# Performance work log

Measured on AMD Instinct MI355X. Metric: run time of the kernel, lower is better.

Reference implementation:

```python
import jax, jax.numpy as jnp
import numpy as np

MAX_SPAN_LENGTH = 4


def setup_inputs() -> dict:
    key = jax.random.key(0)
    ks = jax.random.split(key, 6)
    B, S, H, E = 8, 2048, 768, 32
    hidden_states = jax.random.normal(ks[0], (B, S, H), jnp.float32)
    topic_vector = jax.random.normal(ks[1], (B, H), jnp.float32)
    text_mask = jnp.ones((B, S), dtype=bool)
    length_embedding = jax.random.normal(ks[2], (MAX_SPAN_LENGTH + 1, E), jnp.float32) * 0.02
    W1 = jax.random.normal(ks[3], (3 * H + E, H), jnp.float32) * 0.02
    b1 = jnp.zeros((H,), jnp.float32)
    W2 = jax.random.normal(ks[4], (H, 1), jnp.float32) * 0.02
    b2 = jnp.zeros((1,), jnp.float32)
    return {"hidden_states": hidden_states, "topic_vector": topic_vector,
            "text_mask": text_mask, "length_embedding": length_embedding,
            "W1": W1, "b1": b1, "W2": W2, "b2": b2}


def reference(hidden_states, topic_vector, text_mask, length_embedding, W1, b1, W2, b2):
    B, S, H = hidden_states.shape
    L = MAX_SPAN_LENGTH
    NEG = jnp.float32(-jnp.inf)

    # Static span grid (text_mask is full): span k = (start, start+off), off in [0, L)
    offs = jnp.arange(L)
    starts = jnp.repeat(jnp.arange(S), L)          # [N] with N = S*L
    ends = starts + jnp.tile(offs, S)              # [N]
    valid = ends < S                               # pad spans running off the end
    ends_c = jnp.minimum(ends, S - 1)
    lengths = jnp.tile(offs + 1, S)                # [N] in [1, L]

    start_v = hidden_states[:, starts, :]          # [B,N,H] gather span starts
    end_v = hidden_states[:, ends_c, :]            # [B,N,H] gather span ends
    len_v = length_embedding[lengths]              # [N,E]
    N = starts.shape[0]
    topic = jnp.broadcast_to(topic_vector[:, None, :], (B, N, H))
    feats = jnp.concatenate(
        [topic, start_v, end_v, jnp.broadcast_to(len_v[None], (B, N, len_v.shape[-1]))],
        axis=-1)                                   # [B,N,3H+E]

    h = jax.nn.gelu(feats @ W1 + b1, approximate=False)   # [B,N,H]
    span_scores = (h @ W2)[..., 0] + b2[0]                 # [B,N]
    span_scores = jnp.where(valid[None, :], span_scores, NEG)

    # Project span scores back to tokens via masked max over covering spans
    tok = jnp.arange(S)
    cover = (tok[None, :] >= starts[:, None]) & (tok[None, :] <= ends_c[:, None])  # [N,S]
    token_scores = jnp.max(
        jnp.where(cover[None, :, :], span_scores[:, :, None], NEG), axis=1)       # [B,S]
    token_scores = jnp.where(text_mask, token_scores, NEG)
    return token_scores, span_scores
```

## Files before the change

kernel.cpp:

```cpp
#include <hip/hip_runtime.h>
#include <math.h>

#define B 8
#define S 2048
#define H 768
#define E 32
#define L 4
#define M (B*S)
#define NCOL (2*H)
#define K 768

#define NEG_SENTINEL (-1.0e30f)

typedef float v4f __attribute__((ext_vector_type(4)));
typedef short v8s __attribute__((ext_vector_type(8)));
typedef _Float16 v8h __attribute__((ext_vector_type(8)));
typedef _Float16 v4h __attribute__((ext_vector_type(4)));

__device__ __forceinline__ void bfsplit(float f, unsigned short& h, unsigned short& l) {
  unsigned u = __float_as_uint(f);
  unsigned r = u + 0x7FFF + ((u >> 16) & 1);
  h = (unsigned short)(r >> 16);
  float fh = __uint_as_float(r & 0xFFFF0000u);
  float fl = f - fh;
  unsigned u2 = __float_as_uint(fl);
  unsigned r2 = u2 + 0x7FFF + ((u2 >> 16) & 1);
  l = (unsigned short)(r2 >> 16);
}
__device__ __forceinline__ void split4(float4 f, uint2& h, uint2& l) {
  unsigned short h0,h1,h2,h3,l0,l1,l2,l3;
  bfsplit(f.x,h0,l0); bfsplit(f.y,h1,l1); bfsplit(f.z,h2,l2); bfsplit(f.w,h3,l3);
  h.x = (unsigned)h0 | ((unsigned)h1 << 16); h.y = (unsigned)h2 | ((unsigned)h3 << 16);
  l.x = (unsigned)l0 | ((unsigned)l1 << 16); l.y = (unsigned)l2 | ((unsigned)l3 << 16);
}

__device__ __forceinline__ float gelu_f(float x) {
  float y  = x * 0.70710678118654752f;
  float ay = fabsf(y);
  float t  = __builtin_amdgcn_rcpf(fmaf(0.3275911f, ay, 1.0f));
  float poly = t * fmaf(t, fmaf(t, fmaf(t, fmaf(t, 1.061405429f, -1.453152027f),
                                        1.421413741f), -0.284496736f), 0.254829592f);
  float e  = __expf(-y * y);
  float er = 1.0f - poly * e;
  er = __builtin_copysignf(er, y);
  return 0.5f * x * (1.0f + er);
}


#define SPLITA_BLOCKS 6144
#define CONVW_BLOCKS 288
#define MISC_BLOCKS 36
#define TOPICW_BLOCKS 768

__global__ __launch_bounds__(256) void prep(
    const float* __restrict__ A, const float* __restrict__ W1,
    const float* __restrict__ lenemb, const float* __restrict__ b1,
    _Float16* __restrict__ Af, _Float16* __restrict__ Wf,
    float* __restrict__ topicW, float* __restrict__ lenbase)
{
  __shared__ float t[64][65];
  int bx = blockIdx.x;
  if (bx < SPLITA_BLOCKS) {
    int c = bx * 256 + threadIdx.x;
    int mr = c & 15;
    int cell = c >> 4;
    int kc = cell % 96;
    int m16 = cell / 96;
    int m = m16 * 16 + mr;
    int k0 = kc * 8;
    float4 f0 = *(const float4*)(A + (size_t)m * K + k0);
    float4 f1 = *(const float4*)(A + (size_t)m * K + k0 + 4);
    v8h hv;
    hv[0] = (_Float16)f0.x; hv[1] = (_Float16)f0.y;
    hv[2] = (_Float16)f0.z; hv[3] = (_Float16)f0.w;
    hv[4] = (_Float16)f1.x; hv[5] = (_Float16)f1.y;
    hv[6] = (_Float16)f1.z; hv[7] = (_Float16)f1.w;
    *(v8h*)(Af + (size_t)c * 8) = hv;
  } else if (bx < SPLITA_BLOCKS + CONVW_BLOCKS) {
    int blk = bx - SPLITA_BLOCKS;
    int kb = blk % (K / 64);
    int nb = blk / (K / 64);
    int k0 = kb * 64, n0 = nb * 64;
    int tn = threadIdx.x & 63, tk = threadIdx.x >> 6;
    int n = n0 + tn;
    const float* src = (n < H) ? (W1 + (size_t)(H + k0) * H + n)
                               : (W1 + (size_t)(2 * H + k0) * H + (n - H));
    #pragma unroll
    for (int s = 0; s < 16; s++) {
      int kk = tk + s * 4;
      t[kk][tn] = src[(size_t)kk * H];
    }
    __syncthreads();
    int tkk = threadIdx.x & 63, tnn = threadIdx.x >> 6;
    #pragma unroll
    for (int s = 0; s < 16; s++) {
      int nn = tnn + s * 4;
      float v = t[tkk][nn];
      int n_g = n0 + nn;
      int kk_g = k0 + tkk;
      size_t go = ((size_t)((n_g >> 4) * 96 + (kk_g >> 3)) * 16 + (n_g & 15)) * 8
                + (kk_g & 7);
      Wf[go] = (_Float16)v;
    }
  } else {
    int idx = (bx - SPLITA_BLOCKS - CONVW_BLOCKS) * 256 + threadIdx.x;
    if (idx < L * H) {
      int l = idx / H, h = idx % H;
      float s = b1[h];
      const float* le = lenemb + (size_t)(l + 1) * E;
      #pragma unroll
      for (int e = 0; e < E; e++)
        s = fmaf(le[e], W1[(size_t)(3 * H + e) * H + h], s);
      lenbase[idx] = s;
    } else if (idx < L * H + B * H) {
      topicW[idx - L * H] = 0.f;
    }
  }
}

__global__ __launch_bounds__(256) void gemm_mfma(
    const _Float16* __restrict__ Af, const _Float16* __restrict__ Wf,
    const float* __restrict__ topic, const float* __restrict__ W1,
    float* __restrict__ topicW,
    _Float16* __restrict__ P, _Float16* __restrict__ Q)
{
  __shared__ float red[4][64];
  int tid = threadIdx.x, lane = tid & 63, wv = tid >> 6;
  int f = blockIdx.x;

  if (f >= (M / 128) * (NCOL / 128)) {
    int tw = f - (M / 128) * (NCOL / 128);
    int b = tw / 96;
    int r = tw % 96;
    int h0 = (r / 8) * 64;
    int kc0 = (r % 8) * 96;
    int hcol = tid & 63, ksub = tid >> 6;
    const float* tp = topic + (size_t)b * H;
    float s = 0.f;
    #pragma unroll
    for (int i = 0; i < 24; i++) {
      int k = kc0 + ksub * 24 + i;
      s = fmaf(tp[k], W1[(size_t)k * H + h0 + hcol], s);
    }
    red[ksub][hcol] = s;
    __syncthreads();
    if (tid < 64) {
      float tot = red[0][tid] + red[1][tid] + red[2][tid] + red[3][tid];
      atomicAdd(&topicW[(size_t)b * H + h0 + tid], tot);
    }
    return;
  }

  int xcd = f & 7, g = f >> 3;
  int mb = xcd * 16 + (g / 12);
  int nb = g % 12;
  int wm = (wv >> 1) * 64, wn = (wv & 1) * 64;
  int kg = lane >> 4, fr = lane & 15;

  int aoff[4], boff[4];
  #pragma unroll
  for (int i = 0; i < 4; i++) {
    aoff[i] = ((mb * 8 + (wm >> 4) + i) * 96) * 128 + lane * 8;
    boff[i] = ((nb * 8 + (wn >> 4) + i) * 96) * 128 + lane * 8;
  }

  v4f acc[4][4];
  #pragma unroll
  for (int i = 0; i < 4; i++)
    #pragma unroll
    for (int j = 0; j < 4; j++) { v4f z = {0.f,0.f,0.f,0.f}; acc[i][j] = z; }

  v8h a[2][4], b[2][4];

  #define LOADF(BUF, IT)                                                       \
    { int ko = (IT) * 512;                                                     \
      _Pragma("unroll")                                                        \
      for (int i = 0; i < 4; i++) {                                            \
        a[BUF][i] = *(const v8h*)(Af + aoff[i] + ko);                          \
        b[BUF][i] = *(const v8h*)(Wf + boff[i] + ko);                          \
      } }

  #define COMPUTE(BUF)                                                         \
    { _Pragma("unroll")                                                        \
      for (int j = 0; j < 4; j++)                                              \
        _Pragma("unroll")                                                      \
        for (int i = 0; i < 4; i++)                                            \
          acc[i][j] = __builtin_amdgcn_mfma_f32_16x16x32_f16(                  \
              a[BUF][i], b[BUF][j], acc[i][j], 0, 0, 0); }

  LOADF(0, 0);
  for (int ith = 0; ith < 12; ith++) {
    LOADF(1, 2 * ith + 1);
    COMPUTE(0);
    int itn = (2 * ith + 2 < 24) ? (2 * ith + 2) : 0;
    LOADF(0, itn);
    COMPUTE(1);
  }
  #undef LOADF
  #undef COMPUTE

  int m0 = mb * 128, n0 = nb * 128;
  _Float16* outB = (nb < 6) ? P : Q;
  int cb = (nb < 6) ? n0 : (n0 - H);
  #pragma unroll
  for (int i = 0; i < 4; i++) {
    int row0 = m0 + wm + i * 16 + kg * 4;
    #pragma unroll
    for (int j = 0; j < 4; j++) {
      int col = cb + wn + j * 16 + fr;
      #pragma unroll
      for (int r = 0; r < 4; r++)
        outB[(size_t)(row0 + r) * H + col] = (_Float16)acc[i][j][r];
    }
  }
}


__global__ __launch_bounds__(256) void combine(
    const _Float16* __restrict__ P, const _Float16* __restrict__ Q,
    const float* __restrict__ topicW, const float* __restrict__ lenbase,
    const float* __restrict__ W2, const float* __restrict__ b2,
    float* __restrict__ spanOut)
{
  int tid = threadIdx.x, lane = tid & 63, wv = tid >> 6;
  int siteBase = blockIdx.x * 16;
  int b = siteBase >> 11;
  int c0 = 4 * lane;
  float4 w2v[3], bv[4][3];
  #pragma unroll
  for (int j = 0; j < 3; j++) {
    w2v[j] = *(const float4*)(W2 + c0 + 256 * j);
    float4 tv = *(const float4*)(topicW + (size_t)b * H + c0 + 256 * j);
    #pragma unroll
    for (int l = 0; l < L; l++) {
      float4 lv = *(const float4*)(lenbase + (size_t)l * H + c0 + 256 * j);
      bv[l][j].x = tv.x + lv.x; bv[l][j].y = tv.y + lv.y;
      bv[l][j].z = tv.z + lv.z; bv[l][j].w = tv.w + lv.w;
    }
  }
  float bb2 = b2[0];

  #pragma unroll
  for (int si = 0; si < 4; si++) {
    int site = siteBase + wv * 4 + si;
    int s = site & (S - 1);
    const _Float16* Prow = P + (size_t)site * H;
    float4 p[3];
    #pragma unroll
    for (int j = 0; j < 3; j++) {
      v4h ph = *(const v4h*)(Prow + c0 + 256 * j);
      p[j].x = (float)ph[0]; p[j].y = (float)ph[1];
      p[j].z = (float)ph[2]; p[j].w = (float)ph[3];
    }
    float acc[4];
    #pragma unroll
    for (int l = 0; l < L; l++) {
      int e = min(s + l, S - 1);
      const _Float16* Qrow = Q + ((size_t)(b * S + e)) * H;
      float a = 0.f;
      #pragma unroll
      for (int j = 0; j < 3; j++) {
        v4h qh = *(const v4h*)(Qrow + c0 + 256 * j);
        a = fmaf(gelu_f(bv[l][j].x + p[j].x + (float)qh[0]), w2v[j].x, a);
        a = fmaf(gelu_f(bv[l][j].y + p[j].y + (float)qh[1]), w2v[j].y, a);
        a = fmaf(gelu_f(bv[l][j].z + p[j].z + (float)qh[2]), w2v[j].z, a);
        a = fmaf(gelu_f(bv[l][j].w + p[j].w + (float)qh[3]), w2v[j].w, a);
      }
      acc[l] = a;
    }
    #pragma unroll
    for (int off = 32; off; off >>= 1)
      #pragma unroll
      for (int l = 0; l < L; l++) acc[l] += __shfl_xor(acc[l], off, 64);
    if (lane == 0) {
      #pragma unroll
      for (int l = 0; l < L; l++) {
        float v = (s + l < S) ? (acc[l] + bb2) : NEG_SENTINEL;
        spanOut[(size_t)b * (S * L) + s * L + l] = v;
      }
    }
  }
}

__global__ void token_max(const float* __restrict__ spanOut,
                          float* __restrict__ tokenOut)
{
  int idx = blockIdx.x * 256 + threadIdx.x;
  if (idx >= B * S) return;
  int b = idx >> 11, t = idx & (S - 1);
  float m = -INFINITY;
  int slo = max(t - (L - 1), 0);
  for (int sb = slo; sb <= t; sb++)
    for (int l = t - sb; l < L; l++)
      m = fmaxf(m, spanOut[(size_t)b * (S * L) + sb * L + l]);
  tokenOut[idx] = m;
}


__global__ __launch_bounds__(256) void conv_w_old(
    const float* __restrict__ W1,
    unsigned short* __restrict__ Wh, unsigned short* __restrict__ Wl)
{
  __shared__ float t[64][65];
  int kb = blockIdx.x % (K / 64);
  int nb = blockIdx.x / (K / 64);
  int k0 = kb * 64, n0 = nb * 64;
  int tn = threadIdx.x & 63, tk = threadIdx.x >> 6;
  int n = n0 + tn;
  const float* src = (n < H) ? (W1 + (size_t)(H + k0) * H + n)
                             : (W1 + (size_t)(2 * H + k0) * H + (n - H));
  #pragma unroll
  for (int s = 0; s < 16; s++) {
    int kk = tk + s * 4;
    t[kk][tn] = src[(size_t)kk * H];
  }
  __syncthreads();
  int tkk = threadIdx.x & 63, tnn = threadIdx.x >> 6;
  #pragma unroll
  for (int s = 0; s < 16; s++) {
    int nn = tnn + s * 4;
    float v = t[tkk][nn];
    unsigned short hi, lo;
    bfsplit(v, hi, lo);
    size_t go = (size_t)(n0 + nn) * K + k0 + tkk;
    Wh[go] = hi; Wl[go] = lo;
  }
}

__global__ __launch_bounds__(256) void gemm_old(
    const float* __restrict__ A,
    const unsigned short* __restrict__ Wh,
    const unsigned short* __restrict__ Wl,
    float* __restrict__ P, float* __restrict__ Q)
{
  __shared__ __align__(16) unsigned short Ah_t[128 * 32];
  __shared__ __align__(16) unsigned short Al_t[128 * 32];
  __shared__ __align__(16) unsigned short Bh_t[128 * 32];
  __shared__ __align__(16) unsigned short Bl_t[128 * 32];

  int tid = threadIdx.x;
  int lane = tid & 63, wv = tid >> 6;
  int n0 = blockIdx.x * 128;
  int m0 = blockIdx.y * 128;
  int sr = tid >> 1;
  int sc = (tid & 1) * 16;
  const float* Ap = A + (size_t)(m0 + sr) * K + sc;
  const unsigned short* Bph = Wh + (size_t)(n0 + sr) * K + sc;
  const unsigned short* Bpl = Wl + (size_t)(n0 + sr) * K + sc;
  int wm = (wv >> 1) * 64;
  int wn = (wv & 1) * 64;
  int kg = lane >> 4;
  int fr = lane & 15;

  v4f acc[4][4];
  #pragma unroll
  for (int i = 0; i < 4; i++)
    #pragma unroll
    for (int j = 0; j < 4; j++) { v4f z = {0.f,0.f,0.f,0.f}; acc[i][j] = z; }

  for (int k0 = 0; k0 < K; k0 += 32) {
    float4 a0 = *(const float4*)(Ap + k0);
    float4 a1 = *(const float4*)(Ap + k0 + 4);
    float4 a2 = *(const float4*)(Ap + k0 + 8);
    float4 a3 = *(const float4*)(Ap + k0 + 12);
    uint4 bh0 = *(const uint4*)(Bph + k0);
    uint4 bh1 = *(const uint4*)(Bph + k0 + 8);
    uint4 bl0 = *(const uint4*)(Bpl + k0);
    uint4 bl1 = *(const uint4*)(Bpl + k0 + 8);
    __syncthreads();
    uint2 h0,h1,h2,h3, l0,l1,l2,l3;
    split4(a0,h0,l0); split4(a1,h1,l1); split4(a2,h2,l2); split4(a3,h3,l3);
    uint4 H0 = {h0.x,h0.y,h1.x,h1.y}, H1 = {h2.x,h2.y,h3.x,h3.y};
    uint4 L0 = {l0.x,l0.y,l1.x,l1.y}, L1 = {l2.x,l2.y,l3.x,l3.y};
    *(uint4*)&Ah_t[sr*32 + sc]     = H0;
    *(uint4*)&Ah_t[sr*32 + sc + 8] = H1;
    *(uint4*)&Al_t[sr*32 + sc]     = L0;
    *(uint4*)&Al_t[sr*32 + sc + 8] = L1;
    *(uint4*)&Bh_t[sr*32 + sc]     = bh0;
    *(uint4*)&Bh_t[sr*32 + sc + 8] = bh1;
    *(uint4*)&Bl_t[sr*32 + sc]     = bl0;
    *(uint4*)&Bl_t[sr*32 + sc + 8] = bl1;
    __syncthreads();
    v8s ah[4], al[4], bh[4], bl[4];
    #pragma unroll
    for (int i = 0; i < 4; i++) {
      ah[i] = *(v8s*)&Ah_t[(wm + i*16 + fr)*32 + kg*8];
      al[i] = *(v8s*)&Al_t[(wm + i*16 + fr)*32 + kg*8];
      bh[i] = *(v8s*)&Bh_t[(wn + i*16 + fr)*32 + kg*8];
      bl[i] = *(v8s*)&Bl_t[(wn + i*16 + fr)*32 + kg*8];
    }
    #pragma unroll
    for (int i = 0; i < 4; i++)
      #pragma unroll
      for (int j = 0; j < 4; j++) {
        acc[i][j] = __builtin_amdgcn_mfma_f32_16x16x32_bf16(ah[i], bh[j], acc[i][j], 0, 0, 0);
        acc[i][j] = __builtin_amdgcn_mfma_f32_16x16x32_bf16(ah[i], bl[j], acc[i][j], 0, 0, 0);
        acc[i][j] = __builtin_amdgcn_mfma_f32_16x16x32_bf16(al[i], bh[j], acc[i][j], 0, 0, 0);
      }
  }
  float* outB = (n0 < H) ? P : Q;
  int cb = (n0 < H) ? n0 : (n0 - H);
  #pragma unroll
  for (int i = 0; i < 4; i++) {
    int row0 = m0 + wm + i*16 + kg*4;
    #pragma unroll
    for (int j = 0; j < 4; j++) {
      int col = cb + wn + j*16 + fr;
      #pragma unroll
      for (int r = 0; r < 4; r++)
        outB[(size_t)(row0 + r) * H + col] = acc[i][j][r];
    }
  }
}

__global__ void compute_base(const float* __restrict__ topic,
                             const float* __restrict__ lenemb,
                             const float* __restrict__ W1,
                             const float* __restrict__ b1,
                             float* __restrict__ base)
{
  int idx = blockIdx.x * 256 + threadIdx.x;
  if (idx >= B * L * H) return;
  int h = idx % H;
  int bl = idx / H;
  int l = bl % L;
  int b = bl / L;
  float sacc = b1[h];
  const float* t = topic + b * H;
  for (int k = 0; k < H; k++)
    sacc = fmaf(t[k], W1[(size_t)k * H + h], sacc);
  const float* le = lenemb + (l + 1) * E;
  for (int e = 0; e < E; e++)
    sacc = fmaf(le[e], W1[(size_t)(3 * H + e) * H + h], sacc);
  base[idx] = sacc;
}

__global__ __launch_bounds__(256) void combine_f32(
    const float* __restrict__ P, const float* __restrict__ Q,
    const float* __restrict__ base,
    const float* __restrict__ W2, const float* __restrict__ b2,
    float* __restrict__ spanOut)
{
  int tid = threadIdx.x, lane = tid & 63, wv = tid >> 6;
  int siteBase = blockIdx.x * 16;
  int b = siteBase >> 11;
  int c0 = 4 * lane;
  float4 w2v[3], bv[4][3];
  #pragma unroll
  for (int j = 0; j < 3; j++) {
    w2v[j] = *(const float4*)(W2 + c0 + 256 * j);
    #pragma unroll
    for (int l = 0; l < L; l++)
      bv[l][j] = *(const float4*)(base + ((size_t)(b * L + l)) * H + c0 + 256 * j);
  }
  float bb2 = b2[0];

  #pragma unroll
  for (int si = 0; si < 4; si++) {
    int site = siteBase + wv * 4 + si;
    int s = site & (S - 1);
    const float* Prow = P + (size_t)site * H;
    float4 p[3];
    #pragma unroll
    for (int j = 0; j < 3; j++) p[j] = *(const float4*)(Prow + c0 + 256 * j);
    float acc[4];
    #pragma unroll
    for (int l = 0; l < L; l++) {
      int e = min(s + l, S - 1);
      const float* Qrow = Q + ((size_t)(b * S + e)) * H;
      float a = 0.f;
      #pragma unroll
      for (int j = 0; j < 3; j++) {
        float4 q = *(const float4*)(Qrow + c0 + 256 * j);
        a = fmaf(gelu_f(bv[l][j].x + p[j].x + q.x), w2v[j].x, a);
        a = fmaf(gelu_f(bv[l][j].y + p[j].y + q.y), w2v[j].y, a);
        a = fmaf(gelu_f(bv[l][j].z + p[j].z + q.z), w2v[j].z, a);
        a = fmaf(gelu_f(bv[l][j].w + p[j].w + q.w), w2v[j].w, a);
      }
      acc[l] = a;
    }
    #pragma unroll
    for (int off = 32; off; off >>= 1)
      #pragma unroll
      for (int l = 0; l < L; l++) acc[l] += __shfl_xor(acc[l], off, 64);
    if (lane == 0) {
      #pragma unroll
      for (int l = 0; l < L; l++) {
        float v = (s + l < S) ? (acc[l] + bb2) : NEG_SENTINEL;
        spanOut[(size_t)b * (S * L) + s * L + l] = v;
      }
    }
  }
}

extern "C" void kernel_launch(void* const* d_in, const int* in_sizes, int n_in,
                              void* d_out, int out_size, void* d_ws, size_t ws_size,
                              hipStream_t stream) {
  const float* hidden = (const float*)d_in[0];
  const float* topic  = (const float*)d_in[1];
  const float* lenemb = (const float*)d_in[3];
  const float* W1     = (const float*)d_in[4];
  const float* b1     = (const float*)d_in[5];
  const float* W2     = (const float*)d_in[6];
  const float* b2     = (const float*)d_in[7];

  float* out = (float*)d_out;
  float* tokenOut = out;
  float* spanOut  = out + B * S;

  size_t need = (size_t)(2 * M * H + M * K + NCOL * K) * 2
              + (size_t)(B * H + L * H) * 4;

  if (ws_size >= need) {
    _Float16* Pm = (_Float16*)d_ws;
    _Float16* Qm = Pm + (size_t)M * H;
    _Float16* Af = Qm + (size_t)M * H;
    _Float16* Wf = Af + (size_t)M * K;
    float* topicW  = (float*)(Wf + (size_t)NCOL * K);
    float* lenbase = topicW + (size_t)B * H;

    prep<<<SPLITA_BLOCKS + CONVW_BLOCKS + MISC_BLOCKS, 256, 0, stream>>>(
        hidden, W1, lenemb, b1, Af, Wf, topicW, lenbase);
    gemm_mfma<<<(M / 128) * (NCOL / 128) + TOPICW_BLOCKS, 256, 0, stream>>>(
        Af, Wf, topic, W1, topicW, Pm, Qm);
    combine<<<(B * S) / 16, 256, 0, stream>>>(Pm, Qm, topicW, lenbase, W2, b2, spanOut);
    token_max<<<(B * S + 255) / 256, 256, 0, stream>>>(spanOut, tokenOut);
  } else {
    float* Pm = (float*)d_ws;
    float* Qm = Pm + (size_t)M * H;
    unsigned short* Wh = (unsigned short*)(Qm + (size_t)M * H);
    unsigned short* Wl = Wh + (size_t)NCOL * K;
    float* base = (float*)(Wl + (size_t)NCOL * K);

    conv_w_old<<<(K / 64) * (NCOL / 64), 256, 0, stream>>>(W1, Wh, Wl);
    compute_base<<<(B * L * H + 255) / 256, 256, 0, stream>>>(topic, lenemb, W1, b1, base);
    gemm_old<<<dim3(NCOL / 128, M / 128), 256, 0, stream>>>(hidden, Wh, Wl, Pm, Qm);
    combine_f32<<<(B * S) / 16, 256, 0, stream>>>(Pm, Qm, base, W2, b2, spanOut);
    token_max<<<(B * S + 255) / 256, 256, 0, stream>>>(spanOut, tokenOut);
  }
}
```

Before: 192.2 us.

## Permute GEMM output columns for packed stores and reuse Q rows in combine

```diff
diff --git a/kernel.cpp b/kernel.cpp
--- a/kernel.cpp
+++ b/kernel.cpp
@@ -16,6 +16,10 @@
 typedef short v8s __attribute__((ext_vector_type(8)));
 typedef _Float16 v8h __attribute__((ext_vector_type(8)));
 typedef _Float16 v4h __attribute__((ext_vector_type(4)));
+
+__device__ __forceinline__ int cperm_true(int cp) {
+  return (cp & ~63) | (((cp & 3) << 4) | ((cp >> 2) & 15));
+}
 
 __device__ __forceinline__ void bfsplit(float f, unsigned short& h, unsigned short& l) {
   unsigned u = __float_as_uint(f);
@@ -49,14 +53,16 @@
 
 #define SPLITA_BLOCKS 6144
 #define CONVW_BLOCKS 288
-#define MISC_BLOCKS 36
+#define MISC_BLOCKS 39
 #define TOPICW_BLOCKS 768
 
 __global__ __launch_bounds__(256) void prep(
     const float* __restrict__ A, const float* __restrict__ W1,
     const float* __restrict__ lenemb, const float* __restrict__ b1,
+    const float* __restrict__ W2,
     _Float16* __restrict__ Af, _Float16* __restrict__ Wf,
-    float* __restrict__ topicW, float* __restrict__ lenbase)
+    float* __restrict__ topicW, float* __restrict__ lenbase,
+    float* __restrict__ W2p)
 {
   __shared__ float t[64][65];
   int bx = blockIdx.x;
@@ -105,7 +111,8 @@
   } else {
     int idx = (bx - SPLITA_BLOCKS - CONVW_BLOCKS) * 256 + threadIdx.x;
     if (idx < L * H) {
-      int l = idx / H, h = idx % H;
+      int l = idx / H, cp = idx % H;
+      int h = cperm_true(cp);
       float s = b1[h];
       const float* le = lenemb + (size_t)(l + 1) * E;
       #pragma unroll
@@ -114,11 +121,14 @@
       lenbase[idx] = s;
     } else if (idx < L * H + B * H) {
       topicW[idx - L * H] = 0.f;
-    }
-  }
-}
-
-__global__ __launch_bounds__(256) void gemm_mfma(
+    } else if (idx < L * H + B * H + H) {
+      int cp = idx - L * H - B * H;
+      W2p[cp] = W2[cperm_true(cp)];
+    }
+  }
+}
+
+__global__ __launch_bounds__(256, 2) void gemm_mfma(
     const _Float16* __restrict__ Af, const _Float16* __restrict__ Wf,
     const float* __restrict__ topic, const float* __restrict__ W1,
     float* __restrict__ topicW,
@@ -145,8 +155,9 @@
     red[ksub][hcol] = s;
     __syncthreads();
     if (tid < 64) {
+      int cpo = ((tid & 15) << 2) | (tid >> 4);
       float tot = red[0][tid] + red[1][tid] + red[2][tid] + red[3][tid];
-      atomicAdd(&topicW[(size_t)b * H + h0 + tid], tot);
+      atomicAdd(&topicW[(size_t)b * H + h0 + cpo], tot);
     }
     return;
   }
@@ -170,7 +181,7 @@
     #pragma unroll
     for (int j = 0; j < 4; j++) { v4f z = {0.f,0.f,0.f,0.f}; acc[i][j] = z; }
 
-  v8h a[2][4], b[2][4];
+  v8h a[3][4], b[3][4];
 
   #define LOADF(BUF, IT)                                                       \
     { int ko = (IT) * 512;                                                     \
@@ -181,20 +192,28 @@
       } }
 
   #define COMPUTE(BUF)                                                         \
-    { _Pragma("unroll")                                                        \
+    { __builtin_amdgcn_s_setprio(1);                                           \
+      _Pragma("unroll")                                                        \
       for (int j = 0; j < 4; j++)                                              \
         _Pragma("unroll")                                                      \
         for (int i = 0; i < 4; i++)                                            \
           acc[i][j] = __builtin_amdgcn_mfma_f32_16x16x32_f16(                  \
-              a[BUF][i], b[BUF][j], acc[i][j], 0, 0, 0); }
+              a[BUF][i], b[BUF][j], acc[i][j], 0, 0, 0);                       \
+      __builtin_amdgcn_s_setprio(0); }
 
   LOADF(0, 0);
-  for (int ith = 0; ith < 12; ith++) {
-    LOADF(1, 2 * ith + 1);
+  LOADF(1, 1);
+  #pragma unroll
+  for (int o = 0; o < 8; o++) {
+    int i2 = (3 * o + 2) % 24;
+    int i3 = (3 * o + 3) % 24;
+    int i4 = (3 * o + 4) % 24;
+    LOADF(2, i2);
     COMPUTE(0);
-    int itn = (2 * ith + 2 < 24) ? (2 * ith + 2) : 0;
-    LOADF(0, itn);
+    LOADF(0, i3);
     COMPUTE(1);
+    LOADF(1, i4);
+    COMPUTE(2);
   }
   #undef LOADF
   #undef COMPUTE
@@ -202,15 +221,18 @@
   int m0 = mb * 128, n0 = nb * 128;
   _Float16* outB = (nb < 6) ? P : Q;
   int cb = (nb < 6) ? n0 : (n0 - H);
+  int cbase = cb + wn + fr * 4;
   #pragma unroll
   for (int i = 0; i < 4; i++) {
     int row0 = m0 + wm + i * 16 + kg * 4;
     #pragma unroll
-    for (int j = 0; j < 4; j++) {
-      int col = cb + wn + j * 16 + fr;
-      #pragma unroll
-      for (int r = 0; r < 4; r++)
-        outB[(size_t)(row0 + r) * H + col] = (_Float16)acc[i][j][r];
+    for (int r = 0; r < 4; r++) {
+      v4h pk;
+      pk[0] = (_Float16)acc[i][0][r];
+      pk[1] = (_Float16)acc[i][1][r];
+      pk[2] = (_Float16)acc[i][2][r];
+      pk[3] = (_Float16)acc[i][3][r];
+      *(v4h*)(outB + (size_t)(row0 + r) * H + cbase) = pk;
     }
   }
 }
@@ -219,64 +241,81 @@
 __global__ __launch_bounds__(256) void combine(
     const _Float16* __restrict__ P, const _Float16* __restrict__ Q,
     const float* __restrict__ topicW, const float* __restrict__ lenbase,
-    const float* __restrict__ W2, const float* __restrict__ b2,
+    const float* __restrict__ W2p, const float* __restrict__ b2,
     float* __restrict__ spanOut)
 {
   int tid = threadIdx.x, lane = tid & 63, wv = tid >> 6;
   int siteBase = blockIdx.x * 16;
   int b = siteBase >> 11;
+  int gs0 = siteBase + wv * 4;
+  int s0 = gs0 & (S - 1);
+  int gmax = (b + 1) * S - 1;
   int c0 = 4 * lane;
-  float4 w2v[3], bv[4][3];
+  float bb2 = b2[0];
+
+  float acc[4][4];
+  #pragma unroll
+  for (int si = 0; si < 4; si++)
+    #pragma unroll
+    for (int l = 0; l < L; l++) acc[si][l] = 0.f;
+
   #pragma unroll
   for (int j = 0; j < 3; j++) {
-    w2v[j] = *(const float4*)(W2 + c0 + 256 * j);
-    float4 tv = *(const float4*)(topicW + (size_t)b * H + c0 + 256 * j);
+    int co = c0 + 256 * j;
+    float4 w2 = *(const float4*)(W2p + co);
+    float4 tv = *(const float4*)(topicW + (size_t)b * H + co);
+    float4 bv[4];
     #pragma unroll
     for (int l = 0; l < L; l++) {
-      float4 lv = *(const float4*)(lenbase + (size_t)l * H + c0 + 256 * j);
-      bv[l][j].x = tv.x + lv.x; bv[l][j].y = tv.y + lv.y;
-      bv[l][j].z = tv.z + lv.z; bv[l][j].w = tv.w + lv.w;
-    }
-  }
-  float bb2 = b2[0];
-
-  #pragma unroll
-  for (int si = 0; si < 4; si++) {
-    int site = siteBase + wv * 4 + si;
-    int s = site & (S - 1);
-    const _Float16* Prow = P + (size_t)site * H;
-    float4 p[3];
-    #pragma unroll
-    for (int j = 0; j < 3; j++) {
-      v4h ph = *(const v4h*)(Prow + c0 + 256 * j);
-      p[j].x = (float)ph[0]; p[j].y = (float)ph[1];
-      p[j].z = (float)ph[2]; p[j].w = (float)ph[3];
-    }
-    float acc[4];
-    #pragma unroll
-    for (int l = 0; l < L; l++) {
-      int e = min(s + l, S - 1);
-      const _Float16* Qrow = Q + ((size_t)(b * S + e)) * H;
-      float a = 0.f;
-      #pragma unroll
-      for (int j = 0; j < 3; j++) {
-        v4h qh = *(const v4h*)(Qrow + c0 + 256 * j);
-        a = fmaf(gelu_f(bv[l][j].x + p[j].x + (float)qh[0]), w2v[j].x, a);
-        a = fmaf(gelu_f(bv[l][j].y + p[j].y + (float)qh[1]), w2v[j].y, a);
-        a = fmaf(gelu_f(bv[l][j].z + p[j].z + (float)qh[2]), w2v[j].z, a);
-        a = fmaf(gelu_f(bv[l][j].w + p[j].w + (float)qh[3]), w2v[j].w, a);
+      float4 lv = *(const float4*)(lenbase + (size_t)l * H + co);
+      bv[l].x = tv.x + lv.x; bv[l].y = tv.y + lv.y;
+      bv[l].z = tv.z + lv.z; bv[l].w = tv.w + lv.w;
+    }
+    float4 p[4], q[7];
+    #pragma unroll
+    for (int si = 0; si < 4; si++) {
+      v4h ph = *(const v4h*)(P + (size_t)(gs0 + si) * H + co);
+      p[si].x = (float)ph[0]; p[si].y = (float)ph[1];
+      p[si].z = (float)ph[2]; p[si].w = (float)ph[3];
+    }
+    #pragma unroll
+    for (int r = 0; r < 7; r++) {
+      int grow = gs0 + r; if (grow > gmax) grow = gmax;
+      v4h qh = *(const v4h*)(Q + (size_t)grow * H + co);
+      q[r].x = (float)qh[0]; q[r].y = (float)qh[1];
+      q[r].z = (float)qh[2]; q[r].w = (float)qh[3];
+    }
+    #pragma unroll
+    for (int si = 0; si < 4; si++) {
+      #pragma unroll
+      for (int l = 0; l < L; l++) {
+        int r = si + l;
+        float a0 = acc[si][l];
+        a0 = fmaf(gelu_f(bv[l].x + p[si].x + q[r].x), w2.x, a0);
+        a0 = fmaf(gelu_f(bv[l].y + p[si].y + q[r].y), w2.y, a0);
+        a0 = fmaf(gelu_f(bv[l].z + p[si].z + q[r].z), w2.z, a0);
+        a0 = fmaf(gelu_f(bv[l].w + p[si].w + q[r].w), w2.w, a0);
+        acc[si][l] = a0;
       }
-      acc[l] = a;
-    }
-    #pragma unroll
-    for (int off = 32; off; off >>= 1)
-      #pragma unroll
-      for (int l = 0; l < L; l++) acc[l] += __shfl_xor(acc[l], off, 64);
-    if (lane == 0) {
+    }
+  }
+
+  #pragma unroll
+  for (int off = 32; off; off >>= 1)
+    #pragma unroll
+    for (int si = 0; si < 4; si++)
+      #pragma unroll
+      for (int l = 0; l < L; l++)
+        acc[si][l] += __shfl_xor(acc[si][l], off, 64);
+
+  if (lane == 0) {
+    #pragma unroll
+    for (int si = 0; si < 4; si++) {
+      int s = s0 + si;
       #pragma unroll
       for (int l = 0; l < L; l++) {
-        float v = (s + l < S) ? (acc[l] + bb2) : NEG_SENTINEL;
-        spanOut[(size_t)b * (S * L) + s * L + l] = v;
+        float v = (s + l < S) ? (acc[si][l] + bb2) : NEG_SENTINEL;
+        spanOut[(size_t)b * (S * L) + (size_t)s * L + l] = v;
       }
     }
   }
@@ -509,7 +548,7 @@
   float* spanOut  = out + B * S;
 
   size_t need = (size_t)(2 * M * H + M * K + NCOL * K) * 2
-              + (size_t)(B * H + L * H) * 4;
+              + (size_t)(B * H + L * H + H) * 4;
 
   if (ws_size >= need) {
     _Float16* Pm = (_Float16*)d_ws;
@@ -518,12 +557,13 @@
     _Float16* Wf = Af + (size_t)M * K;
     float* topicW  = (float*)(Wf + (size_t)NCOL * K);
     float* lenbase = topicW + (size_t)B * H;
+    float* W2p     = lenbase + (size_t)L * H;
 
     prep<<<SPLITA_BLOCKS + CONVW_BLOCKS + MISC_BLOCKS, 256, 0, stream>>>(
-        hidden, W1, lenemb, b1, Af, Wf, topicW, lenbase);
+        hidden, W1, lenemb, b1, W2, Af, Wf, topicW, lenbase, W2p);
     gemm_mfma<<<(M / 128) * (NCOL / 128) + TOPICW_BLOCKS, 256, 0, stream>>>(
         Af, Wf, topic, W1, topicW, Pm, Qm);
-    combine<<<(B * S) / 16, 256, 0, stream>>>(Pm, Qm, topicW, lenbase, W2, b2, spanOut);
+    combine<<<(B * S) / 16, 256, 0, stream>>>(Pm, Qm, topicW, lenbase, W2p, b2, spanOut);
     token_max<<<(B * S + 255) / 256, 256, 0, stream>>>(spanOut, tokenOut);
   } else {
     float* Pm = (float*)d_ws;
```

Measured after the change: 177.2 us. 1.08x faster.
